# Optimization experiments

Measured on AMD Instinct MI355X. Metric: run time of the kernel, lower is better.

## Reference

```python
import jax, jax.numpy as jnp
import numpy as np

B, S, H = 1, 2048, 4608
NH, NKV, HD = 36, 4, 128
GROUP = NH // NKV  # 9
ROPE_THETA = 100000.0
SLIDING_WINDOW = 1024


def _rope_tables(seq_len, head_dim):
    inv_freq = 1.0 / (ROPE_THETA ** (jnp.arange(0, head_dim, 2, dtype=jnp.float32) / head_dim))
    ang = jnp.arange(seq_len, dtype=jnp.float32)[:, None] * inv_freq[None, :]  # [S, HD/2]
    emb = jnp.concatenate([ang, ang], axis=-1)  # [S, HD]
    return jnp.cos(emb), jnp.sin(emb)


def setup_inputs() -> dict:
    key = jax.random.key(0)
    ks = jax.random.split(key, 10)
    std = 0.02
    cos_table, sin_table = _rope_tables(S, HD)
    return {
        "hidden_states": jax.random.normal(ks[0], (B, S, H), jnp.float32),
        "position_ids": jnp.broadcast_to(jnp.arange(S, dtype=jnp.int64)[None, :], (B, S)),
        "cos_table": cos_table,
        "sin_table": sin_table,
        "q_w": jax.random.normal(ks[1], (NH * HD, H), jnp.float32) * std,
        "q_b": jax.random.normal(ks[2], (NH * HD,), jnp.float32) * std,
        "k_w": jax.random.normal(ks[3], (NKV * HD, H), jnp.float32) * std,
        "k_b": jax.random.normal(ks[4], (NKV * HD,), jnp.float32) * std,
        "v_w": jax.random.normal(ks[5], (NKV * HD, H), jnp.float32) * std,
        "v_b": jax.random.normal(ks[6], (NKV * HD,), jnp.float32) * std,
        "o_w": jax.random.normal(ks[7], (H, NH * HD), jnp.float32) * std,
        "o_b": jax.random.normal(ks[8], (H,), jnp.float32) * std,
        "sliding_window": SLIDING_WINDOW,
    }


def _rotate_half(x):
    x1, x2 = jnp.split(x, 2, axis=-1)
    return jnp.concatenate([-x2, x1], axis=-1)


def reference(hidden_states, position_ids, cos_table, sin_table,
              q_w, q_b, k_w, k_b, v_w, v_b, o_w, o_b, sliding_window):
    bsz, q_len, _ = hidden_states.shape
    scaling = HD ** -0.5

    q = (hidden_states @ q_w.T + q_b).reshape(bsz, q_len, NH, HD)
    k = (hidden_states @ k_w.T + k_b).reshape(bsz, q_len, NKV, HD)
    v = (hidden_states @ v_w.T + v_b).reshape(bsz, q_len, NKV, HD)

    # RoPE with explicit cos/sin, unsqueeze_dim=2 ('bsnd' layout)
    cos = cos_table[position_ids][:, :, None, :]  # [B, S, 1, HD]
    sin = sin_table[position_ids][:, :, None, :]
    q = q * cos + _rotate_half(q) * sin
    k = k * cos + _rotate_half(k) * sin

    # GQA: group Q heads per KV head
    qg = q.reshape(bsz, q_len, NKV, GROUP, HD)
    logits = jnp.einsum('bqgrd,bkgd->bgrqk', qg, k) * scaling  # [B, NKV, GROUP, S, S]

    # causal + sliding-window mask: attend where k <= q and q - k < window
    idx = jnp.arange(q_len)
    mask = (idx[:, None] >= idx[None, :]) & (idx[:, None] - idx[None, :] < sliding_window)
    logits = jnp.where(mask[None, None, None, :, :], logits, jnp.finfo(logits.dtype).min)

    probs = jax.nn.softmax(logits, axis=-1)
    attn = jnp.einsum('bgrqk,bkgd->bqgrd', probs, v).reshape(bsz, q_len, NH * HD)
    return attn @ o_w.T + o_b
```

## Files before the change

### kernel.cpp

```cpp
#include <hip/hip_runtime.h>
#include <stdint.h>

typedef __attribute__((ext_vector_type(8))) __bf16 bf16x8;
typedef __attribute__((ext_vector_type(4))) float f32x4;
typedef __attribute__((ext_vector_type(8))) unsigned short u16x8;
typedef __attribute__((ext_vector_type(4))) unsigned short u16x4;

#define SEQ 2048
#define HID 4608
#define NQKV 5632
#define NHEAD 36
#define NKVH 4
#define HDIM 128
#define WINDOW 1024

__device__ __forceinline__ unsigned short f2b(float f) {
    unsigned u = __builtin_bit_cast(unsigned, f);
    u += 0x7fffu + ((u >> 16) & 1u);
    return (unsigned short)(u >> 16);
}
__device__ __forceinline__ float b2f(unsigned short h) {
    unsigned u = ((unsigned)h) << 16;
    return __builtin_bit_cast(float, u);
}

#define GLD16(gp, lp) __builtin_amdgcn_global_load_lds( \
    (const __attribute__((address_space(1))) void*)(gp), \
    (__attribute__((address_space(3))) void*)(lp), 16, 0, 0)

#define VMCNT8() asm volatile("s_waitcnt vmcnt(8)" ::: "memory")
#define VMCNT7() asm volatile("s_waitcnt vmcnt(7)" ::: "memory")
#define VMCNT5() asm volatile("s_waitcnt vmcnt(5)" ::: "memory")
#define VMCNT4() asm volatile("s_waitcnt vmcnt(4)" ::: "memory")
#define VMCNT0() asm volatile("s_waitcnt vmcnt(0)" ::: "memory")
#define BARRIER() asm volatile("s_barrier" ::: "memory")

__global__ __launch_bounds__(256) void conv_all_kernel(
    const float* __restrict__ s0, unsigned short* __restrict__ d0, int n0,
    const float* __restrict__ s1, unsigned short* __restrict__ d1, int n1,
    const float* __restrict__ s2, unsigned short* __restrict__ d2, int n2,
    const float* __restrict__ s3, unsigned short* __restrict__ d3, int n3)
{
    int total = n0 + n1 + n2 + n3;
    int stride = gridDim.x * blockDim.x;
    for (int i = blockIdx.x * blockDim.x + threadIdx.x; i < total; i += stride) {
        const float* src; unsigned short* dst; int j = i;
        if (j < n0) { src = s0; dst = d0; }
        else if ((j -= n0) < n1) { src = s1; dst = d1; }
        else if ((j -= n1) < n2) { src = s2; dst = d2; }
        else { j -= n2; src = s3; dst = d3; }
        float4 v = ((const float4*)src)[j];
        ushort4 o;
        o.x = f2b(v.x); o.y = f2b(v.y); o.z = f2b(v.z); o.w = f2b(v.w);
        ((ushort4*)dst)[j] = o;
    }
}

__global__ __launch_bounds__(512, 2) void gemm256_kernel(
    const unsigned short* __restrict__ A,
    const unsigned short* __restrict__ W,
    void* __restrict__ out,
    const float* __restrict__ b0, const float* __restrict__ b1, const float* __restrict__ b2,
    int N, int K, int GX, int GB, int outf32,
    const float* __restrict__ cw_src, unsigned short* __restrict__ cw_dst, int cw_n4)
{
    const int tid = threadIdx.x;
    const int o = blockIdx.x;

    if (o >= GB) {
        int cb = o - GB, ncb = gridDim.x - GB;
        int stride = ncb * 512;
        for (int i = cb * 512 + tid; i < cw_n4; i += stride) {
            float4 v = ((const float4*)cw_src)[i];
            ushort4 u;
            u.x = f2b(v.x); u.y = f2b(v.y); u.z = f2b(v.z); u.w = f2b(v.w);
            ((ushort4*)cw_dst)[i] = u;
        }
        return;
    }

    __shared__ alignas(16) unsigned short ldsA[2][256 * 64];
    __shared__ alignas(16) unsigned short ldsB[2][256 * 64];

    const int w = tid >> 6, lane = tid & 63;
    const int r16 = lane & 15, kg = lane >> 4;
    const int wm = w >> 2, wn = w & 3;

    const int cpx = GB >> 3;
    const int id = (o & 7) * cpx + (o >> 3);
    const int bx = id % GX, by = id / GX;
    const int row0 = by * 256, col0 = bx * 256;

    const int lr = lane >> 3;
    const int lc = lane & 7;
    const int cg = lc ^ lr;
    const unsigned short* Abase = A + (size_t)row0 * K;
    const unsigned short* Wbase = W + (size_t)col0 * K;

    auto STG = [&](const unsigned short* Mat, unsigned short* ldsSlot, int hf, int kb) {
#pragma unroll
        for (int j = 0; j < 2; ++j) {
            int row = hf * 128 + (w * 2 + j) * 8 + lr;
            GLD16(Mat + (size_t)row * K + kb + cg * 8,
                  (char*)ldsSlot + hf * 16384 + (w * 2 + j) * 1024);
        }
    };

    const int NITER = K >> 7;
    f32x4 acc[8][4] = {};
    const int swz = r16 & 7;

    bf16x8 af[4][2], bfA[2][2], bfB[2][2];

#define DSR_A(mh, Sl) \
_Pragma("unroll") for (int mi = 0; mi < 4; ++mi) \
_Pragma("unroll") for (int kh = 0; kh < 2; ++kh) \
    af[mi][kh] = *(const bf16x8*)((Sl) + (wm * 128 + (mh) * 64 + mi * 16 + r16) * 64 + ((kh * 4 + kg) ^ swz) * 8);
#define DSR_B(nh, Sl, BF) \
_Pragma("unroll") for (int ni = 0; ni < 2; ++ni) \
_Pragma("unroll") for (int kh = 0; kh < 2; ++kh) \
    BF[ni][kh] = *(const bf16x8*)((Sl) + (wn * 64 + (nh) * 32 + ni * 16 + r16) * 64 + ((kh * 4 + kg) ^ swz) * 8);
#define MFMA_Q(mh, nh, BF) \
    asm volatile("s_waitcnt lgkmcnt(0)" ::: "memory"); \
    __builtin_amdgcn_sched_barrier(0); \
    __builtin_amdgcn_s_setprio(1); \
_Pragma("unroll") for (int mi = 0; mi < 4; ++mi) \
_Pragma("unroll") for (int ni = 0; ni < 2; ++ni) \
_Pragma("unroll") for (int kh = 0; kh < 2; ++kh) \
    acc[(mh) * 4 + mi][(nh) * 2 + ni] = __builtin_amdgcn_mfma_f32_16x16x32_bf16(af[mi][kh], BF[ni][kh], acc[(mh) * 4 + mi][(nh) * 2 + ni], 0, 0, 0); \
    __builtin_amdgcn_s_setprio(0); \
    __builtin_amdgcn_sched_barrier(0);

    STG(Abase, ldsA[0], 0, 0);  STG(Abase, ldsA[0], 1, 0);
    STG(Wbase, ldsB[0], 0, 0);  STG(Wbase, ldsB[0], 1, 0);
    STG(Abase, ldsA[1], 0, 64); STG(Abase, ldsA[1], 1, 64);
    STG(Wbase, ldsB[1], 0, 64); STG(Wbase, ldsB[1], 1, 64);
    VMCNT0();
    BARRIER();

    for (int i = 0; i < NITER; ++i) {
        const unsigned short* A0 = ldsA[0];
        const unsigned short* B0 = ldsB[0];
        const unsigned short* A1 = ldsA[1];
        const unsigned short* B1 = ldsB[1];
        const bool st = (i + 1 < NITER);
        const int kb0 = (i + 1) * 128;
        const int kb1 = kb0 + 64;

        DSR_A(0, A0); DSR_B(0, B0, bfA);
        BARRIER();
        MFMA_Q(0, 0, bfA);
        BARRIER();
        DSR_B(1, B0, bfB);
        BARRIER();
        MFMA_Q(0, 1, bfB);
        BARRIER();
        DSR_A(1, A0);
        if (st) STG(Wbase, ldsB[0], 0, kb0);
        BARRIER();
        MFMA_Q(1, 1, bfB);
        BARRIER();
        if (st) { STG(Abase, ldsA[0], 0, kb0); VMCNT4(); } else { VMCNT0(); }
        BARRIER();
        MFMA_Q(1, 0, bfA);
        BARRIER();
        DSR_A(0, A1); DSR_B(0, B1, bfA);
        if (st) STG(Abase, ldsA[0], 1, kb0);
        BARRIER();
        MFMA_Q(0, 0, bfA);
        BARRIER();
        DSR_B(1, B1, bfB);
        if (st) STG(Wbase, ldsB[0], 1, kb0);
        BARRIER();
        MFMA_Q(0, 1, bfB);
        BARRIER();
        DSR_A(1, A1);
        if (st) { STG(Wbase, ldsB[1], 0, kb1); STG(Wbase, ldsB[1], 1, kb1); }
        BARRIER();
        MFMA_Q(1, 1, bfB);
        BARRIER();
        if (st) { STG(Abase, ldsA[1], 0, kb1); STG(Abase, ldsA[1], 1, kb1); VMCNT8(); }
        BARRIER();
        MFMA_Q(1, 0, bfA);
        BARRIER();
    }

    if (!outf32) {
        unsigned short* O = (unsigned short*)out;
#pragma unroll
        for (int m = 0; m < 8; ++m)
#pragma unroll
            for (int n = 0; n < 4; ++n)
#pragma unroll
                for (int r = 0; r < 4; ++r) {
                    int row = row0 + wm * 128 + m * 16 + kg * 4 + r;
                    int col = col0 + wn * 64 + n * 16 + r16;
                    float bias = (col < HID) ? b0[col]
                               : (col < HID + 512 ? b1[col - HID] : b2[col - HID - 512]);
                    O[(size_t)row * N + col] = f2b(acc[m][n][r] + bias);
                }
    } else {
        float* O = (float*)out;
#pragma unroll
        for (int m = 0; m < 8; ++m)
#pragma unroll
            for (int n = 0; n < 4; ++n)
#pragma unroll
                for (int r = 0; r < 4; ++r) {
                    int row = row0 + wm * 128 + m * 16 + kg * 4 + r;
                    int col = col0 + wn * 64 + n * 16 + r16;
                    O[(size_t)row * N + col] = acc[m][n][r] + b0[col];
                }
    }
#undef DSR_A
#undef DSR_B
#undef MFMA_Q
}

__global__ __launch_bounds__(512, 1) void gemm192_kernel(
    const unsigned short* __restrict__ A,
    const unsigned short* __restrict__ W,
    float* __restrict__ out,
    const float* __restrict__ b0,
    int N, int K, int GX)
{
    __shared__ alignas(16) unsigned short ldsA[2][256 * 64];
    __shared__ alignas(16) unsigned short ldsB[2][192 * 64];

    const int tid = threadIdx.x;
    const int w = tid >> 6, lane = tid & 63;
    const int r16 = lane & 15, kg = lane >> 4;
    const int wm = w >> 2, wn = w & 3;

    const int cpx = gridDim.x >> 3;
    const int o = blockIdx.x;
    const int id = (o & 7) * cpx + (o >> 3);
    const int bx = id % GX, by = id / GX;
    const int row0 = by * 256, col0 = bx * 192;

    const int lr = lane >> 3;
    const int lc = lane & 7;
    const int cg = lc ^ lr;
    const unsigned short* Abase = A + (size_t)row0 * K;
    const unsigned short* Wbase = W + (size_t)col0 * K;

    auto STGA = [&](unsigned short* slot, int hf, int kb) {
#pragma unroll
        for (int j = 0; j < 2; ++j) {
            int row = hf * 128 + (w * 2 + j) * 8 + lr;
            GLD16(Abase + (size_t)row * K + kb + cg * 8,
                  (char*)slot + hf * 16384 + (w * 2 + j) * 1024);
        }
    };
    auto STGB = [&](unsigned short* slot, int j3, int kb) {
        int row = j3 * 64 + w * 8 + lr;
        GLD16(Wbase + (size_t)row * K + kb + cg * 8,
              (char*)slot + j3 * 8192 + w * 1024);
    };

    const int NITER = K >> 7;
    f32x4 acc[8][3] = {};
    const int swz = r16 & 7;

    bf16x8 af[4][2], bf2[2][2], bf1[2];

#define DSR_A(mh, Sl) \
_Pragma("unroll") for (int mi = 0; mi < 4; ++mi) \
_Pragma("unroll") for (int kh = 0; kh < 2; ++kh) \
    af[mi][kh] = *(const bf16x8*)((Sl) + (wm * 128 + (mh) * 64 + mi * 16 + r16) * 64 + ((kh * 4 + kg) ^ swz) * 8);
#define DSR_B2(Sl) \
_Pragma("unroll") for (int ni = 0; ni < 2; ++ni) \
_Pragma("unroll") for (int kh = 0; kh < 2; ++kh) \
    bf2[ni][kh] = *(const bf16x8*)((Sl) + (wn * 48 + ni * 16 + r16) * 64 + ((kh * 4 + kg) ^ swz) * 8);
#define DSR_B1(Sl) \
_Pragma("unroll") for (int kh = 0; kh < 2; ++kh) \
    bf1[kh] = *(const bf16x8*)((Sl) + (wn * 48 + 32 + r16) * 64 + ((kh * 4 + kg) ^ swz) * 8);
#define MFMA_Q2(mh) \
    asm volatile("s_waitcnt lgkmcnt(0)" ::: "memory"); \
    __builtin_amdgcn_sched_barrier(0); \
    __builtin_amdgcn_s_setprio(1); \
_Pragma("unroll") for (int mi = 0; mi < 4; ++mi) \
_Pragma("unroll") for (int ni = 0; ni < 2; ++ni) \
_Pragma("unroll") for (int kh = 0; kh < 2; ++kh) \
    acc[(mh) * 4 + mi][ni] = __builtin_amdgcn_mfma_f32_16x16x32_bf16(af[mi][kh], bf2[ni][kh], acc[(mh) * 4 + mi][ni], 0, 0, 0); \
    __builtin_amdgcn_s_setprio(0); \
    __builtin_amdgcn_sched_barrier(0);
#define MFMA_Q1(mh) \
    asm volatile("s_waitcnt lgkmcnt(0)" ::: "memory"); \
    __builtin_amdgcn_sched_barrier(0); \
    __builtin_amdgcn_s_setprio(1); \
_Pragma("unroll") for (int mi = 0; mi < 4; ++mi) \
_Pragma("unroll") for (int kh = 0; kh < 2; ++kh) \
    acc[(mh) * 4 + mi][2] = __builtin_amdgcn_mfma_f32_16x16x32_bf16(af[mi][kh], bf1[kh], acc[(mh) * 4 + mi][2], 0, 0, 0); \
    __builtin_amdgcn_s_setprio(0); \
    __builtin_amdgcn_sched_barrier(0);

    STGA(ldsA[0], 0, 0);  STGA(ldsA[0], 1, 0);
    STGB(ldsB[0], 0, 0);  STGB(ldsB[0], 1, 0);  STGB(ldsB[0], 2, 0);
    STGA(ldsA[1], 0, 64); STGA(ldsA[1], 1, 64);
    STGB(ldsB[1], 0, 64); STGB(ldsB[1], 1, 64); STGB(ldsB[1], 2, 64);
    VMCNT0();
    BARRIER();

    for (int i = 0; i < NITER; ++i) {
        const unsigned short* A0 = ldsA[0];
        const unsigned short* B0 = ldsB[0];
        const unsigned short* A1 = ldsA[1];
        const unsigned short* B1 = ldsB[1];
        const bool st = (i + 1 < NITER);
        const int kb0 = (i + 1) * 128;
        const int kb1 = kb0 + 64;

        DSR_A(0, A0); DSR_B2(B0);
        BARRIER();
        MFMA_Q2(0);
        BARRIER();
        DSR_B1(B0);
        BARRIER();
        MFMA_Q1(0);
        BARRIER();
        DSR_A(1, A0);
        if (st) { STGB(ldsB[0], 0, kb0); STGB(ldsB[0], 1, kb0); STGB(ldsB[0], 2, kb0); }
        BARRIER();
        MFMA_Q1(1);
        BARRIER();
        if (st) { STGA(ldsA[0], 0, kb0); VMCNT5(); } else { VMCNT0(); }
        BARRIER();
        MFMA_Q2(1);
        BARRIER();
        DSR_A(0, A1); DSR_B2(B1);
        if (st) STGA(ldsA[0], 1, kb0);
        BARRIER();
        MFMA_Q2(0);
        BARRIER();
        DSR_B1(B1);
        BARRIER();
        MFMA_Q1(0);
        BARRIER();
        DSR_A(1, A1);
        if (st) { STGB(ldsB[1], 0, kb1); STGB(ldsB[1], 1, kb1); STGB(ldsB[1], 2, kb1);
                  STGA(ldsA[1], 0, kb1); }
        BARRIER();
        MFMA_Q1(1);
        BARRIER();
        if (st) { STGA(ldsA[1], 1, kb1); VMCNT7(); }
        BARRIER();
        MFMA_Q2(1);
        BARRIER();
    }

#pragma unroll
    for (int m = 0; m < 8; ++m)
#pragma unroll
        for (int n = 0; n < 3; ++n)
#pragma unroll
            for (int r = 0; r < 4; ++r) {
                int row = row0 + wm * 128 + m * 16 + kg * 4 + r;
                int col = col0 + wn * 48 + n * 16 + r16;
                out[(size_t)row * N + col] = acc[m][n][r] + b0[col];
            }
#undef DSR_A
#undef DSR_B2
#undef DSR_B1
#undef MFMA_Q2
#undef MFMA_Q1
}

__global__ __launch_bounds__(256) void rope_vt_kernel(unsigned short* __restrict__ qkv,
                                                      const float* __restrict__ cos_t,
                                                      const float* __restrict__ sin_t,
                                                      unsigned short* __restrict__ vtg) {
    const int bid = blockIdx.x;
    if (bid < 5120) {
        int idx = bid * 256 + threadIdx.x;
        int d4 = idx & 15;
        int t2 = idx >> 4;
        int head = t2 % 40;
        int s = t2 / 40;
        int base = head < NHEAD ? head * HDIM : HID + (head - NHEAD) * HDIM;
        size_t off = (size_t)s * NQKV + base + d4 * 4;
        u16x4 xv = *(const u16x4*)(qkv + off);
        u16x4 yv = *(const u16x4*)(qkv + off + 64);
        float4 c = *(const float4*)(cos_t + s * HDIM + d4 * 4);
        float4 sn = *(const float4*)(sin_t + s * HDIM + d4 * 4);
        u16x4 xo, yo;
        float x, y;
        x = b2f(xv[0]); y = b2f(yv[0]); xo[0] = f2b(x * c.x - y * sn.x); yo[0] = f2b(y * c.x + x * sn.x);
        x = b2f(xv[1]); y = b2f(yv[1]); xo[1] = f2b(x * c.y - y * sn.y); yo[1] = f2b(y * c.y + x * sn.y);
        x = b2f(xv[2]); y = b2f(yv[2]); xo[2] = f2b(x * c.z - y * sn.z); yo[2] = f2b(y * c.z + x * sn.z);
        x = b2f(xv[3]); y = b2f(yv[3]); xo[3] = f2b(x * c.w - y * sn.w); yo[3] = f2b(y * c.w + x * sn.w);
        *(u16x4*)(qkv + off) = xo;
        *(u16x4*)(qkv + off + 64) = yo;
    } else {
        __shared__ unsigned short tile[32][36];
        int vb = bid - 5120;
        const int s0 = (vb & 63) * 32;
        const int d0 = ((vb >> 6) & 3) * 32;
        const int kvh = vb >> 8;
        const int lid = threadIdx.x;
        {
            int sl = lid >> 3, dc = (lid & 7) * 4;
            u16x4 v = *(const u16x4*)(qkv + (size_t)(s0 + sl) * NQKV + HID + 512 + kvh * HDIM + d0 + dc);
#pragma unroll
            for (int i = 0; i < 4; ++i) tile[sl][dc + i] = v[i];
        }
        __syncthreads();
        {
            int dl = lid >> 3, sc = (lid & 7) * 4;
            u16x4 v;
#pragma unroll
            for (int i = 0; i < 4; ++i) v[i] = tile[sc + i][dl];
            *(u16x4*)(vtg + (size_t)kvh * HDIM * SEQ + (size_t)(d0 + dl) * SEQ + s0 + sc) = v;
        }
    }
}

#define KSTR 136
#define VSTR 72
#define PSTR 88
__global__ __launch_bounds__(512) void attn_kernel(const unsigned short* __restrict__ qkv,
                                                   const unsigned short* __restrict__ vtg,
                                                   unsigned short* __restrict__ aout)
{
    __shared__ alignas(16) unsigned short Ks[64 * KSTR];
    __shared__ alignas(16) unsigned short Vt[128 * VSTR];
    __shared__ alignas(16) unsigned short Ps[8 * 16 * PSTR];
    const int h = blockIdx.x, qb = blockIdx.y;
    const int q0 = qb * 128;
    const int kvh = h / 9;
    const int tid = threadIdx.x, wid = tid >> 6, lane = tid & 63;
    const int r16 = lane & 15, kg = lane >> 4;
    const int qbase = q0 + wid * 16;
    const unsigned short* vsrc = vtg + (size_t)kvh * HDIM * SEQ;

    bf16x8 qf[4];
    {
        const unsigned short* qrow = qkv + (size_t)(qbase + r16) * NQKV + h * HDIM;
#pragma unroll
        for (int kk = 0; kk < 4; ++kk)
            qf[kk] = *(const bf16x8*)(qrow + kk * 32 + kg * 8);
    }

    f32x4 o[8] = {};
    float mrow[4], lrow[4];
#pragma unroll
    for (int r = 0; r < 4; ++r) { mrow[r] = -1e30f; lrow[r] = 0.f; }

    int lo = q0 - (WINDOW - 1); if (lo < 0) lo = 0; lo &= ~63;
    const int hi = q0 + 64;
    unsigned short* myP = Ps + wid * 16 * PSTR;
    const float scale = 0.08838834764831845f;

    u16x8 kreg[2], vreg[2];
#define PREF(KT) \
_Pragma("unroll") for (int j = 0; j < 2; ++j) { \
        int c = tid + j * 512; \
        int key = c >> 4, dc = c & 15; \
        kreg[j] = *(const u16x8*)(qkv + (size_t)((KT) + key) * NQKV + HID + kvh * HDIM + dc * 8); \
        int d = c >> 3, k8 = (c & 7) * 8; \
        vreg[j] = *(const u16x8*)(vsrc + (size_t)d * SEQ + (KT) + k8); \
    }

    PREF(lo);

    for (int kt = lo; kt <= hi; kt += 64) {
#pragma unroll
        for (int j = 0; j < 2; ++j) {
            int c = tid + j * 512;
            int key = c >> 4, dc = c & 15;
            *(u16x8*)(Ks + key * KSTR + dc * 8) = kreg[j];
            int d = c >> 3, k8 = (c & 7) * 8;
            *(u16x8*)(Vt + d * VSTR + k8) = vreg[j];
        }
        __syncthreads();

        if (kt + 64 <= hi) { PREF(kt + 64); }

        f32x4 sc[4] = {};
#pragma unroll
        for (int t = 0; t < 4; ++t)
#pragma unroll
            for (int kk = 0; kk < 4; ++kk) {
                bf16x8 kf = *(const bf16x8*)(Ks + (t * 16 + r16) * KSTR + kk * 32 + kg * 8);
                sc[t] = __builtin_amdgcn_mfma_f32_16x16x32_bf16(qf[kk], kf, sc[t], 0, 0, 0);
            }

        float p[4][4], mt[4];
#pragma unroll
        for (int r = 0; r < 4; ++r) mt[r] = -1e30f;
        const bool fullv = (kt + 63 <= qbase) && (qbase + 15 - kt < WINDOW);
        if (fullv) {
#pragma unroll
            for (int t = 0; t < 4; ++t)
#pragma unroll
                for (int r = 0; r < 4; ++r) {
                    float v = sc[t][r] * scale;
                    p[t][r] = v;
                    mt[r] = fmaxf(mt[r], v);
                }
        } else {
#pragma unroll
            for (int t = 0; t < 4; ++t)
#pragma unroll
                for (int r = 0; r < 4; ++r) {
                    int q = qbase + kg * 4 + r;
                    int key = kt + t * 16 + r16;
                    bool valid = (key <= q) && (q - key < WINDOW);
                    float v = valid ? sc[t][r] * scale : -1e30f;
                    p[t][r] = v;
                    mt[r] = fmaxf(mt[r], v);
                }
        }
#pragma unroll
        for (int mask = 1; mask <= 8; mask <<= 1)
#pragma unroll
            for (int r = 0; r < 4; ++r)
                mt[r] = fmaxf(mt[r], __shfl_xor(mt[r], mask, 64));

        float alpha[4], tsum[4];
#pragma unroll
        for (int r = 0; r < 4; ++r) {
            float mnew = fmaxf(mrow[r], mt[r]);
            alpha[r] = __expf(mrow[r] - mnew);
            mrow[r] = mnew;
            tsum[r] = 0.f;
        }
#pragma unroll
        for (int t = 0; t < 4; ++t)
#pragma unroll
            for (int r = 0; r < 4; ++r) {
                float e = __expf(p[t][r] - mrow[r]);
                p[t][r] = e;
                tsum[r] += e;
            }
#pragma unroll
        for (int mask = 1; mask <= 8; mask <<= 1)
#pragma unroll
            for (int r = 0; r < 4; ++r)
                tsum[r] += __shfl_xor(tsum[r], mask, 64);
#pragma unroll
        for (int r = 0; r < 4; ++r)
            lrow[r] = lrow[r] * alpha[r] + tsum[r];
#pragma unroll
        for (int n = 0; n < 8; ++n)
#pragma unroll
            for (int r = 0; r < 4; ++r)
                o[n][r] = o[n][r] * alpha[r];

#pragma unroll
        for (int t = 0; t < 4; ++t)
#pragma unroll
            for (int r = 0; r < 4; ++r)
                myP[(kg * 4 + r) * PSTR + t * 16 + r16] = f2b(p[t][r]);
        asm volatile("s_waitcnt lgkmcnt(0)" ::: "memory");

#pragma unroll
        for (int kc = 0; kc < 2; ++kc) {
            bf16x8 pa = *(const bf16x8*)(myP + r16 * PSTR + kc * 32 + kg * 8);
#pragma unroll
            for (int n = 0; n < 8; ++n) {
                bf16x8 vb = *(const bf16x8*)(Vt + (n * 16 + r16) * VSTR + kc * 32 + kg * 8);
                o[n] = __builtin_amdgcn_mfma_f32_16x16x32_bf16(pa, vb, o[n], 0, 0, 0);
            }
        }
        BARRIER();
    }
#undef PREF

#pragma unroll
    for (int n = 0; n < 8; ++n)
#pragma unroll
        for (int r = 0; r < 4; ++r) {
            int q = qbase + kg * 4 + r;
            aout[(size_t)q * HID + h * HDIM + n * 16 + r16] = f2b(o[n][r] / lrow[r]);
        }
}

extern "C" void kernel_launch(void* const* d_in, const int* in_sizes, int n_in,
                              void* d_out, int out_size, void* d_ws, size_t ws_size,
                              hipStream_t stream) {
    const float* hidden = (const float*)d_in[0];
    const float* cos_t = (const float*)d_in[2];
    const float* sin_t = (const float*)d_in[3];
    const float* q_w = (const float*)d_in[4];
    const float* q_b = (const float*)d_in[5];
    const float* k_w = (const float*)d_in[6];
    const float* k_b = (const float*)d_in[7];
    const float* v_w = (const float*)d_in[8];
    const float* v_b = (const float*)d_in[9];
    const float* o_w = (const float*)d_in[10];
    const float* o_b = (const float*)d_in[11];

    char* ws = (char*)d_ws;
    unsigned short* hbf  = (unsigned short*)ws;
    unsigned short* attn = hbf;
    unsigned short* wqkv = (unsigned short*)(ws + 18874368);
    unsigned short* vtg  = wqkv;
    unsigned short* wo   = (unsigned short*)(ws + 70778880);
    unsigned short* qkv  = (unsigned short*)(ws + 113246208);

    dim3 blk(256);
    conv_all_kernel<<<4096, blk, 0, stream>>>(
        hidden, hbf,                          (SEQ * HID) / 4,
        q_w,    wqkv,                         (HID * HID) / 4,
        k_w,    wqkv + (size_t)HID * HID,     (512 * HID) / 4,
        v_w,    wqkv + (size_t)5120 * HID,    (512 * HID) / 4);

    gemm256_kernel<<<dim3(256), dim3(512), 0, stream>>>(
        hbf, wqkv, qkv, q_b, k_b, v_b, NQKV, HID, 22, 176, 0,
        o_w, wo, (HID * HID) / 4);
    rope_vt_kernel<<<6144, blk, 0, stream>>>(qkv, cos_t, sin_t, vtg);
    attn_kernel<<<dim3(NHEAD, SEQ / 128), dim3(512), 0, stream>>>(qkv, vtg, attn);
    gemm192_kernel<<<dim3(192), dim3(512), 0, stream>>>(
        attn, wo, (float*)d_out, o_b, HID, HID, 24);
}
```

Measured before the change: 413.4 us.

## Halve output-projection GEMM row tile and attention query tile for more blocks

The output projection GEMM moves from 256x192 tiles with 192 blocks to 128x192 tiles with 384 blocks. Its pipeline becomes simpler, with fused A/B staging per half-K step and a launch bound that allows more blocks per CU. The attention kernel drops from 128 query rows per 512-thread block to 64 rows per 256-thread block, doubling the grid and trimming the extra key tile beyond the diagonal. The aim is better CU coverage and less idle work, at the cost of lower operand reuse per block and more global traffic for weights and K/V.

```diff
diff --git a/kernel.cpp b/kernel.cpp
--- a/kernel.cpp
+++ b/kernel.cpp
@@ -29,7 +29,6 @@
     (__attribute__((address_space(3))) void*)(lp), 16, 0, 0)
 
 #define VMCNT8() asm volatile("s_waitcnt vmcnt(8)" ::: "memory")
-#define VMCNT7() asm volatile("s_waitcnt vmcnt(7)" ::: "memory")
 #define VMCNT5() asm volatile("s_waitcnt vmcnt(5)" ::: "memory")
 #define VMCNT4() asm volatile("s_waitcnt vmcnt(4)" ::: "memory")
 #define VMCNT0() asm volatile("s_waitcnt vmcnt(0)" ::: "memory")
@@ -217,14 +216,14 @@
 #undef MFMA_Q
 }
 
-__global__ __launch_bounds__(512, 1) void gemm192_kernel(
+__global__ __launch_bounds__(512, 4) void gemm_op_kernel(
     const unsigned short* __restrict__ A,
     const unsigned short* __restrict__ W,
     float* __restrict__ out,
     const float* __restrict__ b0,
     int N, int K, int GX)
 {
-    __shared__ alignas(16) unsigned short ldsA[2][256 * 64];
+    __shared__ alignas(16) unsigned short ldsA[2][128 * 64];
     __shared__ alignas(16) unsigned short ldsB[2][192 * 64];
 
     const int tid = threadIdx.x;
@@ -236,7 +235,7 @@
     const int o = blockIdx.x;
     const int id = (o & 7) * cpx + (o >> 3);
     const int bx = id % GX, by = id / GX;
-    const int row0 = by * 256, col0 = bx * 192;
+    const int row0 = by * 128, col0 = bx * 192;
 
     const int lr = lane >> 3;
     const int lc = lane & 7;
@@ -244,126 +243,89 @@
     const unsigned short* Abase = A + (size_t)row0 * K;
     const unsigned short* Wbase = W + (size_t)col0 * K;
 
-    auto STGA = [&](unsigned short* slot, int hf, int kb) {
+    auto STGA = [&](unsigned short* slot, int kb) {
 #pragma unroll
         for (int j = 0; j < 2; ++j) {
-            int row = hf * 128 + (w * 2 + j) * 8 + lr;
+            int row = (w * 2 + j) * 8 + lr;
             GLD16(Abase + (size_t)row * K + kb + cg * 8,
-                  (char*)slot + hf * 16384 + (w * 2 + j) * 1024);
+                  (char*)slot + (w * 2 + j) * 1024);
         }
     };
-    auto STGB = [&](unsigned short* slot, int j3, int kb) {
-        int row = j3 * 64 + w * 8 + lr;
-        GLD16(Wbase + (size_t)row * K + kb + cg * 8,
-              (char*)slot + j3 * 8192 + w * 1024);
+    auto STGB = [&](unsigned short* slot, int kb) {
+#pragma unroll
+        for (int j3 = 0; j3 < 3; ++j3) {
+            int row = j3 * 64 + w * 8 + lr;
+            GLD16(Wbase + (size_t)row * K + kb + cg * 8,
+                  (char*)slot + j3 * 8192 + w * 1024);
+        }
     };
 
     const int NITER = K >> 7;
-    f32x4 acc[8][3] = {};
+    f32x4 acc[4][3] = {};
     const int swz = r16 & 7;
 
-    bf16x8 af[4][2], bf2[2][2], bf1[2];
-
-#define DSR_A(mh, Sl) \
+    bf16x8 af[4][2], bf[3][2];
+
+#define DSR_AF(Sl) \
 _Pragma("unroll") for (int mi = 0; mi < 4; ++mi) \
 _Pragma("unroll") for (int kh = 0; kh < 2; ++kh) \
-    af[mi][kh] = *(const bf16x8*)((Sl) + (wm * 128 + (mh) * 64 + mi * 16 + r16) * 64 + ((kh * 4 + kg) ^ swz) * 8);
-#define DSR_B2(Sl) \
-_Pragma("unroll") for (int ni = 0; ni < 2; ++ni) \
+    af[mi][kh] = *(const bf16x8*)((Sl) + (wm * 64 + mi * 16 + r16) * 64 + ((kh * 4 + kg) ^ swz) * 8);
+#define DSR_BF(Sl) \
+_Pragma("unroll") for (int ni = 0; ni < 3; ++ni) \
 _Pragma("unroll") for (int kh = 0; kh < 2; ++kh) \
-    bf2[ni][kh] = *(const bf16x8*)((Sl) + (wn * 48 + ni * 16 + r16) * 64 + ((kh * 4 + kg) ^ swz) * 8);
-#define DSR_B1(Sl) \
-_Pragma("unroll") for (int kh = 0; kh < 2; ++kh) \
-    bf1[kh] = *(const bf16x8*)((Sl) + (wn * 48 + 32 + r16) * 64 + ((kh * 4 + kg) ^ swz) * 8);
-#define MFMA_Q2(mh) \
+    bf[ni][kh] = *(const bf16x8*)((Sl) + (wn * 48 + ni * 16 + r16) * 64 + ((kh * 4 + kg) ^ swz) * 8);
+#define MFMA12(half) \
     asm volatile("s_waitcnt lgkmcnt(0)" ::: "memory"); \
     __builtin_amdgcn_sched_barrier(0); \
     __builtin_amdgcn_s_setprio(1); \
-_Pragma("unroll") for (int mi = 0; mi < 4; ++mi) \
-_Pragma("unroll") for (int ni = 0; ni < 2; ++ni) \
+_Pragma("unroll") for (int mi = 0; mi < 2; ++mi) \
+_Pragma("unroll") for (int ni = 0; ni < 3; ++ni) \
 _Pragma("unroll") for (int kh = 0; kh < 2; ++kh) \
-    acc[(mh) * 4 + mi][ni] = __builtin_amdgcn_mfma_f32_16x16x32_bf16(af[mi][kh], bf2[ni][kh], acc[(mh) * 4 + mi][ni], 0, 0, 0); \
+    acc[(half) * 2 + mi][ni] = __builtin_amdgcn_mfma_f32_16x16x32_bf16(af[(half) * 2 + mi][kh], bf[ni][kh], acc[(half) * 2 + mi][ni], 0, 0, 0); \
     __builtin_amdgcn_s_setprio(0); \
     __builtin_amdgcn_sched_barrier(0);
-#define MFMA_Q1(mh) \
-    asm volatile("s_waitcnt lgkmcnt(0)" ::: "memory"); \
-    __builtin_amdgcn_sched_barrier(0); \
-    __builtin_amdgcn_s_setprio(1); \
-_Pragma("unroll") for (int mi = 0; mi < 4; ++mi) \
-_Pragma("unroll") for (int kh = 0; kh < 2; ++kh) \
-    acc[(mh) * 4 + mi][2] = __builtin_amdgcn_mfma_f32_16x16x32_bf16(af[mi][kh], bf1[kh], acc[(mh) * 4 + mi][2], 0, 0, 0); \
-    __builtin_amdgcn_s_setprio(0); \
-    __builtin_amdgcn_sched_barrier(0);
-
-    STGA(ldsA[0], 0, 0);  STGA(ldsA[0], 1, 0);
-    STGB(ldsB[0], 0, 0);  STGB(ldsB[0], 1, 0);  STGB(ldsB[0], 2, 0);
-    STGA(ldsA[1], 0, 64); STGA(ldsA[1], 1, 64);
-    STGB(ldsB[1], 0, 64); STGB(ldsB[1], 1, 64); STGB(ldsB[1], 2, 64);
+
+    STGA(ldsA[0], 0);  STGB(ldsB[0], 0);
+    STGA(ldsA[1], 64); STGB(ldsB[1], 64);
     VMCNT0();
     BARRIER();
 
     for (int i = 0; i < NITER; ++i) {
-        const unsigned short* A0 = ldsA[0];
-        const unsigned short* B0 = ldsB[0];
-        const unsigned short* A1 = ldsA[1];
-        const unsigned short* B1 = ldsB[1];
         const bool st = (i + 1 < NITER);
         const int kb0 = (i + 1) * 128;
         const int kb1 = kb0 + 64;
 
-        DSR_A(0, A0); DSR_B2(B0);
-        BARRIER();
-        MFMA_Q2(0);
-        BARRIER();
-        DSR_B1(B0);
-        BARRIER();
-        MFMA_Q1(0);
-        BARRIER();
-        DSR_A(1, A0);
-        if (st) { STGB(ldsB[0], 0, kb0); STGB(ldsB[0], 1, kb0); STGB(ldsB[0], 2, kb0); }
-        BARRIER();
-        MFMA_Q1(1);
-        BARRIER();
-        if (st) { STGA(ldsA[0], 0, kb0); VMCNT5(); } else { VMCNT0(); }
-        BARRIER();
-        MFMA_Q2(1);
-        BARRIER();
-        DSR_A(0, A1); DSR_B2(B1);
-        if (st) STGA(ldsA[0], 1, kb0);
-        BARRIER();
-        MFMA_Q2(0);
-        BARRIER();
-        DSR_B1(B1);
-        BARRIER();
-        MFMA_Q1(0);
-        BARRIER();
-        DSR_A(1, A1);
-        if (st) { STGB(ldsB[1], 0, kb1); STGB(ldsB[1], 1, kb1); STGB(ldsB[1], 2, kb1);
-                  STGA(ldsA[1], 0, kb1); }
-        BARRIER();
-        MFMA_Q1(1);
-        BARRIER();
-        if (st) { STGA(ldsA[1], 1, kb1); VMCNT7(); }
-        BARRIER();
-        MFMA_Q2(1);
-        BARRIER();
-    }
-
-#pragma unroll
-    for (int m = 0; m < 8; ++m)
+        DSR_AF(ldsA[0]); DSR_BF(ldsB[0]);
+        BARRIER();
+        MFMA12(0);
+        BARRIER();
+        if (st) { STGA(ldsA[0], kb0); STGB(ldsB[0], kb0); VMCNT5(); } else { VMCNT0(); }
+        BARRIER();
+        MFMA12(1);
+        BARRIER();
+        DSR_AF(ldsA[1]); DSR_BF(ldsB[1]);
+        BARRIER();
+        MFMA12(0);
+        BARRIER();
+        if (st) { STGA(ldsA[1], kb1); STGB(ldsB[1], kb1); VMCNT5(); }
+        BARRIER();
+        MFMA12(1);
+        BARRIER();
+    }
+
+#pragma unroll
+    for (int m = 0; m < 4; ++m)
 #pragma unroll
         for (int n = 0; n < 3; ++n)
 #pragma unroll
             for (int r = 0; r < 4; ++r) {
-                int row = row0 + wm * 128 + m * 16 + kg * 4 + r;
+                int row = row0 + wm * 64 + m * 16 + kg * 4 + r;
                 int col = col0 + wn * 48 + n * 16 + r16;
                 out[(size_t)row * N + col] = acc[m][n][r] + b0[col];
             }
-#undef DSR_A
-#undef DSR_B2
-#undef DSR_B1
-#undef MFMA_Q2
-#undef MFMA_Q1
+#undef DSR_AF
+#undef DSR_BF
+#undef MFMA12
 }
 
 __global__ __launch_bounds__(256) void rope_vt_kernel(unsigned short* __restrict__ qkv,
@@ -418,15 +380,15 @@
 #define KSTR 136
 #define VSTR 72
 #define PSTR 88
-__global__ __launch_bounds__(512) void attn_kernel(const unsigned short* __restrict__ qkv,
+__global__ __launch_bounds__(256) void attn_kernel(const unsigned short* __restrict__ qkv,
                                                    const unsigned short* __restrict__ vtg,
                                                    unsigned short* __restrict__ aout)
 {
     __shared__ alignas(16) unsigned short Ks[64 * KSTR];
     __shared__ alignas(16) unsigned short Vt[128 * VSTR];
-    __shared__ alignas(16) unsigned short Ps[8 * 16 * PSTR];
+    __shared__ alignas(16) unsigned short Ps[4 * 16 * PSTR];
     const int h = blockIdx.x, qb = blockIdx.y;
-    const int q0 = qb * 128;
+    const int q0 = qb * 64;
     const int kvh = h / 9;
     const int tid = threadIdx.x, wid = tid >> 6, lane = tid & 63;
     const int r16 = lane & 15, kg = lane >> 4;
@@ -447,14 +409,13 @@
     for (int r = 0; r < 4; ++r) { mrow[r] = -1e30f; lrow[r] = 0.f; }
 
     int lo = q0 - (WINDOW - 1); if (lo < 0) lo = 0; lo &= ~63;
-    const int hi = q0 + 64;
     unsigned short* myP = Ps + wid * 16 * PSTR;
     const float scale = 0.08838834764831845f;
 
-    u16x8 kreg[2], vreg[2];
+    u16x8 kreg[4], vreg[4];
 #define PREF(KT) \
-_Pragma("unroll") for (int j = 0; j < 2; ++j) { \
-        int c = tid + j * 512; \
+_Pragma("unroll") for (int j = 0; j < 4; ++j) { \
+        int c = tid + j * 256; \
         int key = c >> 4, dc = c & 15; \
         kreg[j] = *(const u16x8*)(qkv + (size_t)((KT) + key) * NQKV + HID + kvh * HDIM + dc * 8); \
         int d = c >> 3, k8 = (c & 7) * 8; \
@@ -463,10 +424,10 @@
 
     PREF(lo);
 
-    for (int kt = lo; kt <= hi; kt += 64) {
-#pragma unroll
-        for (int j = 0; j < 2; ++j) {
-            int c = tid + j * 512;
+    for (int kt = lo; kt <= q0; kt += 64) {
+#pragma unroll
+        for (int j = 0; j < 4; ++j) {
+            int c = tid + j * 256;
             int key = c >> 4, dc = c & 15;
             *(u16x8*)(Ks + key * KSTR + dc * 8) = kreg[j];
             int d = c >> 3, k8 = (c & 7) * 8;
@@ -474,7 +435,7 @@
         }
         __syncthreads();
 
-        if (kt + 64 <= hi) { PREF(kt + 64); }
+        if (kt + 64 <= q0) { PREF(kt + 64); }
 
         f32x4 sc[4] = {};
 #pragma unroll
@@ -610,7 +571,7 @@
         hbf, wqkv, qkv, q_b, k_b, v_b, NQKV, HID, 22, 176, 0,
         o_w, wo, (HID * HID) / 4);
     rope_vt_kernel<<<6144, blk, 0, stream>>>(qkv, cos_t, sin_t, vtg);
-    attn_kernel<<<dim3(NHEAD, SEQ / 128), dim3(512), 0, stream>>>(qkv, vtg, attn);
-    gemm192_kernel<<<dim3(192), dim3(512), 0, stream>>>(
+    attn_kernel<<<dim3(NHEAD, SEQ / 64), blk, 0, stream>>>(qkv, vtg, attn);
+    gemm_op_kernel<<<dim3(384), dim3(512), 0, stream>>>(
         attn, wo, (float*)d_out, o_b, HID, HID, 24);
 }
```

Measured after the change: 364.2 us, median of 4. 11.9% less time.
